# Kernel optimization log

Hardware: AMD Instinct MI355X
Metric: run time of the kernel (lower is better)

Reference implementation:

```python
import jax, jax.numpy as jnp
import numpy as np

B, DIN, NS, NF = 2048, 512, 256, 64

def setup_inputs() -> dict:
    key = jax.random.key(0)
    ks = jax.random.split(key, 16)
    s = 0.05
    return {
        'x_i': jax.random.normal(ks[0], (B, DIN), jnp.float32),
        'h_i': jax.random.normal(ks[1], (B, NS), jnp.float32),
        'S_i': jax.random.normal(ks[2], (B, 2, NS, NF), jnp.float32),
        'W_fste': jax.random.normal(ks[3], (DIN + NS, NS), jnp.float32) * s,
        'b_fste': jnp.zeros((NS,), jnp.float32),
        'W_ffreq': jax.random.normal(ks[4], (DIN + NS, NF), jnp.float32) * s,
        'b_ffreq': jnp.zeros((NF,), jnp.float32),
        'W_i': jax.random.normal(ks[5], (DIN + NS, NS), jnp.float32) * s,
        'b_i': jnp.zeros((NS,), jnp.float32),
        'W_c': jax.random.normal(ks[6], (DIN + NS, NS), jnp.float32) * s,
        'b_c': jnp.zeros((NS,), jnp.float32),
        'u_a': jax.random.normal(ks[7], (NF,), jnp.float32) * s,
        'b_a': jnp.zeros((NS,), jnp.float32),
        'W_o': jax.random.normal(ks[8], (DIN + NS + NS, NS), jnp.float32) * s,
        'b_o': jnp.zeros((NS,), jnp.float32),
        't': 3,
    }

def reference(x_i, h_i, S_i, W_fste, b_fste, W_ffreq, b_ffreq, W_i, b_i, W_c, b_c, u_a, b_a, W_o, b_o, t):
    nf = u_a.shape[0]
    # angle = ((arange(nf)*t) % nf) / (nf / (2*pi))  -- matches np precedence in source
    ang = ((jnp.arange(nf, dtype=jnp.float32) * t) % nf) * (2.0 * jnp.pi / nf)
    omega = jnp.stack([jnp.sin(ang), jnp.cos(ang)])[:, None]        # [2,1,nf]
    x_h = jnp.concatenate([x_i, h_i], axis=-1)                      # [B, DIN+NS]
    f_ste = jax.nn.sigmoid(x_h @ W_fste + b_fste)                   # [B,NS]
    f_freq = jax.nn.sigmoid(x_h @ W_ffreq + b_ffreq)                # [B,NF]
    F_t = jnp.einsum('bi,bj->bij', f_ste, f_freq)                   # [B,NS,NF]
    i_dot = jax.nn.sigmoid(x_h @ W_i + b_i)                         # [B,NS]
    c_wave = jnp.tanh(x_h @ W_c + b_c)                              # [B,NS]
    i_c_omega = (i_dot * c_wave)[:, None, :, None] * omega          # [B,2,NS,NF]
    S_next = S_i * F_t[:, None] + i_c_omega                         # [B,2,NS,NF]
    A_i = jnp.sqrt(jnp.sum(S_next ** 2, axis=1))                    # [B,NS,NF]
    c_t = jax.nn.sigmoid(jnp.einsum('bij,j->bi', A_i, u_a) + b_a)   # [B,NS]
    o_i = jax.nn.sigmoid(jnp.concatenate([x_h, c_t], -1) @ W_o + b_o)
    h_next = o_i * c_t
    return h_next, S_next
```

## Files before the change

kernel.cpp:

```cpp
#include <hip/hip_runtime.h>
#include <math.h>

#define BATCH 2048
#define DIN   512
#define NS    256
#define NF    64
#define KG    768
#define NG    832
#define NTOT  1088

__device__ __forceinline__ float sigmoidf_(float x) { return 1.0f / (1.0f + __expf(-x)); }

__global__ __launch_bounds__(256) void gates_gemm(
    const float* __restrict__ x, const float* __restrict__ h,
    const float* __restrict__ Wf, const float* __restrict__ bf,
    const float* __restrict__ Wq, const float* __restrict__ bq,
    const float* __restrict__ Wi, const float* __restrict__ bi,
    const float* __restrict__ Wc, const float* __restrict__ bcg,
    const float* __restrict__ Wo,
    float* __restrict__ gates, float* __restrict__ opart)
{
    __shared__ float As[2][32][68];
    __shared__ float Bs[2][32][68];

    const int nt = blockIdx.x;
    const int mt = blockIdx.y;
    const int t  = threadIdx.x;

    const int n0 = nt * 64;
    const float* Wp; const float* bp; int ld, noff, act;
    if (n0 < 256)      { Wp = Wf; bp = bf;  ld = 256; noff = 0;   act = 0; }
    else if (n0 < 320) { Wp = Wq; bp = bq;  ld = 64;  noff = 256; act = 0; }
    else if (n0 < 576) { Wp = Wi; bp = bi;  ld = 256; noff = 320; act = 0; }
    else if (n0 < 832) { Wp = Wc; bp = bcg; ld = 256; noff = 576; act = 1; }
    else               { Wp = Wo; bp = bf;  ld = 256; noff = 832; act = 2; }
    const int nloc0 = n0 - noff;

    const int tx = t & 15, ty = t >> 4;
    const int m0 = mt * 64;

    const int ar  = t & 63;
    const int ak0 = (t >> 6) * 8;
    const int brow  = t >> 3;
    const int bcol0 = (t & 7) * 8;

    const float* ax = x + (size_t)(m0 + ar) * DIN;
    const float* ah = h + (size_t)(m0 + ar) * NS;

    float acc[4][4] = {};
    float4 a0, a1, b0, b1;

    {
        const int k0 = ak0;
        a0 = *(const float4*)(ax + k0);
        a1 = *(const float4*)(ax + k0 + 4);
        const float* wr = Wp + (size_t)brow * ld + nloc0 + bcol0;
        b0 = *(const float4*)wr; b1 = *(const float4*)(wr + 4);
        As[0][ak0 + 0][ar] = a0.x; As[0][ak0 + 1][ar] = a0.y;
        As[0][ak0 + 2][ar] = a0.z; As[0][ak0 + 3][ar] = a0.w;
        As[0][ak0 + 4][ar] = a1.x; As[0][ak0 + 5][ar] = a1.y;
        As[0][ak0 + 6][ar] = a1.z; As[0][ak0 + 7][ar] = a1.w;
        *(float4*)&Bs[0][brow][bcol0]     = b0;
        *(float4*)&Bs[0][brow][bcol0 + 4] = b1;
    }
    __syncthreads();

    #pragma unroll 1
    for (int tI = 0; tI < 24; ++tI) {
        const int notlast = (tI < 23);
        if (notlast) {
            const int kt = (tI + 1) * 32;
            const int k0 = kt + ak0;
            a0 = (k0 < DIN)     ? *(const float4*)(ax + k0)
                                : *(const float4*)(ah + (k0 - DIN));
            a1 = (k0 + 4 < DIN) ? *(const float4*)(ax + k0 + 4)
                                : *(const float4*)(ah + (k0 + 4 - DIN));
            const float* wr = Wp + (size_t)(kt + brow) * ld + nloc0 + bcol0;
            b0 = *(const float4*)wr; b1 = *(const float4*)(wr + 4);
        }
        const float (*Asb)[68] = As[tI & 1];
        const float (*Bsb)[68] = Bs[tI & 1];
        #pragma unroll
        for (int kk = 0; kk < 32; ++kk) {
            const float4 a = *(const float4*)&Asb[kk][ty * 4];
            const float4 b = *(const float4*)&Bsb[kk][tx * 4];
            const float av[4] = { a.x, a.y, a.z, a.w };
            const float bv[4] = { b.x, b.y, b.z, b.w };
            #pragma unroll
            for (int r = 0; r < 4; ++r)
                #pragma unroll
                for (int c = 0; c < 4; ++c)
                    acc[r][c] = fmaf(av[r], bv[c], acc[r][c]);
        }
        if (notlast) {
            float (*Ad)[68] = As[(tI + 1) & 1];
            float (*Bd)[68] = Bs[(tI + 1) & 1];
            Ad[ak0 + 0][ar] = a0.x; Ad[ak0 + 1][ar] = a0.y;
            Ad[ak0 + 2][ar] = a0.z; Ad[ak0 + 3][ar] = a0.w;
            Ad[ak0 + 4][ar] = a1.x; Ad[ak0 + 5][ar] = a1.y;
            Ad[ak0 + 6][ar] = a1.z; Ad[ak0 + 7][ar] = a1.w;
            *(float4*)&Bd[brow][bcol0]     = b0;
            *(float4*)&Bd[brow][bcol0 + 4] = b1;
        }
        __syncthreads();
    }

    if (act == 2) {
        #pragma unroll
        for (int r = 0; r < 4; ++r) {
            const int m = m0 + ty * 4 + r;
            *(float4*)(opart + (size_t)m * NS + (n0 - 832) + tx * 4) =
                make_float4(acc[r][0], acc[r][1], acc[r][2], acc[r][3]);
        }
    } else {
        const float4 bb = *(const float4*)(bp + nloc0 + tx * 4);
        const float bvv[4] = { bb.x, bb.y, bb.z, bb.w };
        #pragma unroll
        for (int r = 0; r < 4; ++r) {
            const int m = m0 + ty * 4 + r;
            float o[4];
            #pragma unroll
            for (int c = 0; c < 4; ++c) {
                float v = acc[r][c] + bvv[c];
                o[c] = act ? tanhf(v) : sigmoidf_(v);
            }
            *(float4*)(gates + (size_t)m * NG + n0 + tx * 4) =
                make_float4(o[0], o[1], o[2], o[3]);
        }
    }
}

__global__ __launch_bounds__(256) void supdate(
    const float* __restrict__ S, const float* __restrict__ gates,
    const float* __restrict__ ua, const float* __restrict__ ba,
    const int* __restrict__ tptr,
    float* __restrict__ Sout, float* __restrict__ ct)
{
    const int tid = blockIdx.x * 256 + threadIdx.x;
    const int q    = tid & 15;
    const int pair = tid >> 4;
    const int b = pair >> 8, s = pair & 255;
    const int f0 = q * 4;
    const int tv = *tptr;

    const float* grow = gates + (size_t)b * NG;
    const float fste = grow[s];
    const float ic   = grow[320 + s] * grow[576 + s];

    const float4 ff  = *(const float4*)(grow + 256 + f0);
    const float4 ua4 = *(const float4*)(ua + f0);

    const size_t base0 = (((size_t)b * 2 + 0) * NS + s) * NF + f0;
    const size_t base1 = (((size_t)b * 2 + 1) * NS + s) * NF + f0;
    const float4 si0 = *(const float4*)(S + base0);
    const float4 si1 = *(const float4*)(S + base1);

    float fv[4] = { ff.x, ff.y, ff.z, ff.w };
    float uv[4] = { ua4.x, ua4.y, ua4.z, ua4.w };
    float a0[4] = { si0.x, si0.y, si0.z, si0.w };
    float a1[4] = { si1.x, si1.y, si1.z, si1.w };

    float part = 0.0f;
    float o0[4], o1[4];
    #pragma unroll
    for (int j = 0; j < 4; ++j) {
        int f = f0 + j;
        float ang = (float)((f * tv) & (NF - 1)) * (float)(M_PI / 32.0);
        float sn = __sinf(ang), cs = __cosf(ang);
        float F = fste * fv[j];
        float u = a0[j] * F + ic * sn;
        float v = a1[j] * F + ic * cs;
        o0[j] = u; o1[j] = v;
        part += sqrtf(u * u + v * v) * uv[j];
    }
    *(float4*)(Sout + base0) = make_float4(o0[0], o0[1], o0[2], o0[3]);
    *(float4*)(Sout + base1) = make_float4(o1[0], o1[1], o1[2], o1[3]);

    part += __shfl_xor(part, 1);
    part += __shfl_xor(part, 2);
    part += __shfl_xor(part, 4);
    part += __shfl_xor(part, 8);
    if (q == 0) ct[pair] = sigmoidf_(part + ba[s]);
}

__global__ __launch_bounds__(256) void out_gemm(
    const float* __restrict__ ct, const float* __restrict__ opart,
    const float* __restrict__ Wo, const float* __restrict__ bo,
    float* __restrict__ hout)
{
    __shared__ float As[2][32][36];
    __shared__ float Bs[2][32][68];

    const int t  = threadIdx.x;
    const int n0 = blockIdx.x * 64;
    const int m0 = blockIdx.y * 32;
    const int tx = t & 15, ty = t >> 4;

    const int ar  = t & 31;
    const int ak0 = (t >> 5) * 4;
    const int brow  = t >> 3;
    const int bcol0 = (t & 7) * 8;

    const float* Wp = Wo + (size_t)(DIN + NS) * NS;
    const float* act_row = ct + (size_t)(m0 + ar) * NS;

    float acc[2][4] = {};
    float4 a4, b0, b1;

    a4 = *(const float4*)(act_row + ak0);
    {
        const float* wr = Wp + (size_t)brow * NS + n0 + bcol0;
        b0 = *(const float4*)wr; b1 = *(const float4*)(wr + 4);
    }
    As[0][ak0 + 0][ar] = a4.x; As[0][ak0 + 1][ar] = a4.y;
    As[0][ak0 + 2][ar] = a4.z; As[0][ak0 + 3][ar] = a4.w;
    *(float4*)&Bs[0][brow][bcol0]     = b0;
    *(float4*)&Bs[0][brow][bcol0 + 4] = b1;
    __syncthreads();

    #pragma unroll 1
    for (int tI = 0; tI < 8; ++tI) {
        const int notlast = (tI < 7);
        if (notlast) {
            const int kt = (tI + 1) * 32;
            a4 = *(const float4*)(act_row + kt + ak0);
            const float* wr = Wp + (size_t)(kt + brow) * NS + n0 + bcol0;
            b0 = *(const float4*)wr; b1 = *(const float4*)(wr + 4);
        }
        const float (*Asb)[36] = As[tI & 1];
        const float (*Bsb)[68] = Bs[tI & 1];
        #pragma unroll
        for (int kk = 0; kk < 32; ++kk) {
            const float a0v = Asb[kk][ty * 2];
            const float a1v = Asb[kk][ty * 2 + 1];
            const float4 b = *(const float4*)&Bsb[kk][tx * 4];
            acc[0][0] = fmaf(a0v, b.x, acc[0][0]);
            acc[0][1] = fmaf(a0v, b.y, acc[0][1]);
            acc[0][2] = fmaf(a0v, b.z, acc[0][2]);
            acc[0][3] = fmaf(a0v, b.w, acc[0][3]);
            acc[1][0] = fmaf(a1v, b.x, acc[1][0]);
            acc[1][1] = fmaf(a1v, b.y, acc[1][1]);
            acc[1][2] = fmaf(a1v, b.z, acc[1][2]);
            acc[1][3] = fmaf(a1v, b.w, acc[1][3]);
        }
        if (notlast) {
            float (*Ad)[36] = As[(tI + 1) & 1];
            float (*Bd)[68] = Bs[(tI + 1) & 1];
            Ad[ak0 + 0][ar] = a4.x; Ad[ak0 + 1][ar] = a4.y;
            Ad[ak0 + 2][ar] = a4.z; Ad[ak0 + 3][ar] = a4.w;
            *(float4*)&Bd[brow][bcol0]     = b0;
            *(float4*)&Bd[brow][bcol0 + 4] = b1;
        }
        __syncthreads();
    }

    #pragma unroll
    for (int r = 0; r < 2; ++r) {
        const int m = m0 + ty * 2 + r;
        const float4 op = *(const float4*)(opart + (size_t)m * NS + n0 + tx * 4);
        const float4 bb = *(const float4*)(bo + n0 + tx * 4);
        const float4 cv = *(const float4*)(ct + (size_t)m * NS + n0 + tx * 4);
        float4 o;
        o.x = sigmoidf_(acc[r][0] + op.x + bb.x) * cv.x;
        o.y = sigmoidf_(acc[r][1] + op.y + bb.y) * cv.y;
        o.z = sigmoidf_(acc[r][2] + op.z + bb.z) * cv.z;
        o.w = sigmoidf_(acc[r][3] + op.w + bb.w) * cv.w;
        *(float4*)(hout + (size_t)m * NS + n0 + tx * 4) = o;
    }
}

extern "C" void kernel_launch(void* const* d_in, const int* in_sizes, int n_in,
                              void* d_out, int out_size, void* d_ws, size_t ws_size,
                              hipStream_t stream)
{
    const float* x  = (const float*)d_in[0];
    const float* h  = (const float*)d_in[1];
    const float* S  = (const float*)d_in[2];
    const float* Wf = (const float*)d_in[3];
    const float* bf = (const float*)d_in[4];
    const float* Wq = (const float*)d_in[5];
    const float* bq = (const float*)d_in[6];
    const float* Wi = (const float*)d_in[7];
    const float* bi = (const float*)d_in[8];
    const float* Wc = (const float*)d_in[9];
    const float* bc = (const float*)d_in[10];
    const float* ua = (const float*)d_in[11];
    const float* ba = (const float*)d_in[12];
    const float* Wo = (const float*)d_in[13];
    const float* bo = (const float*)d_in[14];
    const int*   tp = (const int*)d_in[15];

    float* gates = (float*)d_ws;
    float* ct    = gates + (size_t)BATCH * NG;
    float* opart = ct + (size_t)BATCH * NS;
    float* hout  = (float*)d_out;
    float* Sout  = hout + (size_t)BATCH * NS;

    gates_gemm<<<dim3(17, 32), 256, 0, stream>>>(x, h, Wf, bf, Wq, bq, Wi, bi, Wc, bc, Wo, gates, opart);
    supdate<<<dim3((BATCH * NS * 16) / 256), 256, 0, stream>>>(S, gates, ua, ba, tp, Sout, ct);
    out_gemm<<<dim3(4, 64), 256, 0, stream>>>(ct, opart, Wo, bo, hout);
}
```

Baseline: 594.1 us.

## Halve gates GEMM tile width and use nontemporal loads/stores for S

The gates GEMM now uses 64x32 tiles with 128-thread blocks, doubling the block count from 544 to 1088 to fill more of the GPU's compute units. The per-thread loaders are reworked so each thread loads 16 A elements and two strided B vectors. The S state update now reads and writes through nontemporal builtins, so the 268MB streaming traffic does not pollute the caches. The narrower tiles lower arithmetic intensity and add redundant A loads across N tiles.

```diff
diff --git a/kernel.cpp b/kernel.cpp
--- a/kernel.cpp
+++ b/kernel.cpp
@@ -9,9 +9,11 @@
 #define NG    832
 #define NTOT  1088
 
+typedef float v4f __attribute__((ext_vector_type(4)));
+
 __device__ __forceinline__ float sigmoidf_(float x) { return 1.0f / (1.0f + __expf(-x)); }
 
-__global__ __launch_bounds__(256) void gates_gemm(
+__global__ __launch_bounds__(128) void gates_gemm(
     const float* __restrict__ x, const float* __restrict__ h,
     const float* __restrict__ Wf, const float* __restrict__ bf,
     const float* __restrict__ Wq, const float* __restrict__ bq,
@@ -21,13 +23,13 @@
     float* __restrict__ gates, float* __restrict__ opart)
 {
     __shared__ float As[2][32][68];
-    __shared__ float Bs[2][32][68];
+    __shared__ float Bs[2][32][36];
 
     const int nt = blockIdx.x;
     const int mt = blockIdx.y;
     const int t  = threadIdx.x;
 
-    const int n0 = nt * 64;
+    const int n0 = nt * 32;
     const float* Wp; const float* bp; int ld, noff, act;
     if (n0 < 256)      { Wp = Wf; bp = bf;  ld = 256; noff = 0;   act = 0; }
     else if (n0 < 320) { Wp = Wq; bp = bq;  ld = 64;  noff = 256; act = 0; }
@@ -36,32 +38,37 @@
     else               { Wp = Wo; bp = bf;  ld = 256; noff = 832; act = 2; }
     const int nloc0 = n0 - noff;
 
-    const int tx = t & 15, ty = t >> 4;
+    const int tx = t & 7, ty = t >> 3;
     const int m0 = mt * 64;
 
     const int ar  = t & 63;
-    const int ak0 = (t >> 6) * 8;
-    const int brow  = t >> 3;
-    const int bcol0 = (t & 7) * 8;
+    const int ak0 = (t >> 6) * 16;
+    const int brow  = t >> 2;
+    const int bcol0 = (t & 3) * 4;
 
     const float* ax = x + (size_t)(m0 + ar) * DIN;
     const float* ah = h + (size_t)(m0 + ar) * NS;
 
     float acc[4][4] = {};
-    float4 a0, a1, b0, b1;
+    float4 a0, a1, a2, a3, b0, b1;
 
     {
-        const int k0 = ak0;
-        a0 = *(const float4*)(ax + k0);
-        a1 = *(const float4*)(ax + k0 + 4);
+        a0 = *(const float4*)(ax + ak0);
+        a1 = *(const float4*)(ax + ak0 + 4);
+        a2 = *(const float4*)(ax + ak0 + 8);
+        a3 = *(const float4*)(ax + ak0 + 12);
         const float* wr = Wp + (size_t)brow * ld + nloc0 + bcol0;
-        b0 = *(const float4*)wr; b1 = *(const float4*)(wr + 4);
-        As[0][ak0 + 0][ar] = a0.x; As[0][ak0 + 1][ar] = a0.y;
-        As[0][ak0 + 2][ar] = a0.z; As[0][ak0 + 3][ar] = a0.w;
-        As[0][ak0 + 4][ar] = a1.x; As[0][ak0 + 5][ar] = a1.y;
-        As[0][ak0 + 6][ar] = a1.z; As[0][ak0 + 7][ar] = a1.w;
-        *(float4*)&Bs[0][brow][bcol0]     = b0;
-        *(float4*)&Bs[0][brow][bcol0 + 4] = b1;
+        b0 = *(const float4*)wr; b1 = *(const float4*)(wr + 16);
+        As[0][ak0 +  0][ar] = a0.x; As[0][ak0 +  1][ar] = a0.y;
+        As[0][ak0 +  2][ar] = a0.z; As[0][ak0 +  3][ar] = a0.w;
+        As[0][ak0 +  4][ar] = a1.x; As[0][ak0 +  5][ar] = a1.y;
+        As[0][ak0 +  6][ar] = a1.z; As[0][ak0 +  7][ar] = a1.w;
+        As[0][ak0 +  8][ar] = a2.x; As[0][ak0 +  9][ar] = a2.y;
+        As[0][ak0 + 10][ar] = a2.z; As[0][ak0 + 11][ar] = a2.w;
+        As[0][ak0 + 12][ar] = a3.x; As[0][ak0 + 13][ar] = a3.y;
+        As[0][ak0 + 14][ar] = a3.z; As[0][ak0 + 15][ar] = a3.w;
+        *(float4*)&Bs[0][brow][bcol0]      = b0;
+        *(float4*)&Bs[0][brow][bcol0 + 16] = b1;
     }
     __syncthreads();
 
@@ -71,15 +78,16 @@
         if (notlast) {
             const int kt = (tI + 1) * 32;
             const int k0 = kt + ak0;
-            a0 = (k0 < DIN)     ? *(const float4*)(ax + k0)
-                                : *(const float4*)(ah + (k0 - DIN));
-            a1 = (k0 + 4 < DIN) ? *(const float4*)(ax + k0 + 4)
-                                : *(const float4*)(ah + (k0 + 4 - DIN));
+            const float* ap = (k0 < DIN) ? (ax + k0) : (ah + (k0 - DIN));
+            a0 = *(const float4*)(ap);
+            a1 = *(const float4*)(ap + 4);
+            a2 = *(const float4*)(ap + 8);
+            a3 = *(const float4*)(ap + 12);
             const float* wr = Wp + (size_t)(kt + brow) * ld + nloc0 + bcol0;
-            b0 = *(const float4*)wr; b1 = *(const float4*)(wr + 4);
+            b0 = *(const float4*)wr; b1 = *(const float4*)(wr + 16);
         }
         const float (*Asb)[68] = As[tI & 1];
-        const float (*Bsb)[68] = Bs[tI & 1];
+        const float (*Bsb)[36] = Bs[tI & 1];
         #pragma unroll
         for (int kk = 0; kk < 32; ++kk) {
             const float4 a = *(const float4*)&Asb[kk][ty * 4];
@@ -94,13 +102,17 @@
         }
         if (notlast) {
             float (*Ad)[68] = As[(tI + 1) & 1];
-            float (*Bd)[68] = Bs[(tI + 1) & 1];
-            Ad[ak0 + 0][ar] = a0.x; Ad[ak0 + 1][ar] = a0.y;
-            Ad[ak0 + 2][ar] = a0.z; Ad[ak0 + 3][ar] = a0.w;
-            Ad[ak0 + 4][ar] = a1.x; Ad[ak0 + 5][ar] = a1.y;
-            Ad[ak0 + 6][ar] = a1.z; Ad[ak0 + 7][ar] = a1.w;
-            *(float4*)&Bd[brow][bcol0]     = b0;
-            *(float4*)&Bd[brow][bcol0 + 4] = b1;
+            float (*Bd)[36] = Bs[(tI + 1) & 1];
+            Ad[ak0 +  0][ar] = a0.x; Ad[ak0 +  1][ar] = a0.y;
+            Ad[ak0 +  2][ar] = a0.z; Ad[ak0 +  3][ar] = a0.w;
+            Ad[ak0 +  4][ar] = a1.x; Ad[ak0 +  5][ar] = a1.y;
+            Ad[ak0 +  6][ar] = a1.z; Ad[ak0 +  7][ar] = a1.w;
+            Ad[ak0 +  8][ar] = a2.x; Ad[ak0 +  9][ar] = a2.y;
+            Ad[ak0 + 10][ar] = a2.z; Ad[ak0 + 11][ar] = a2.w;
+            Ad[ak0 + 12][ar] = a3.x; Ad[ak0 + 13][ar] = a3.y;
+            Ad[ak0 + 14][ar] = a3.z; Ad[ak0 + 15][ar] = a3.w;
+            *(float4*)&Bd[brow][bcol0]      = b0;
+            *(float4*)&Bd[brow][bcol0 + 16] = b1;
         }
         __syncthreads();
     }
@@ -152,8 +164,8 @@
 
     const size_t base0 = (((size_t)b * 2 + 0) * NS + s) * NF + f0;
     const size_t base1 = (((size_t)b * 2 + 1) * NS + s) * NF + f0;
-    const float4 si0 = *(const float4*)(S + base0);
-    const float4 si1 = *(const float4*)(S + base1);
+    const v4f si0 = __builtin_nontemporal_load((const v4f*)(S + base0));
+    const v4f si1 = __builtin_nontemporal_load((const v4f*)(S + base1));
 
     float fv[4] = { ff.x, ff.y, ff.z, ff.w };
     float uv[4] = { ua4.x, ua4.y, ua4.z, ua4.w };
@@ -161,7 +173,7 @@
     float a1[4] = { si1.x, si1.y, si1.z, si1.w };
 
     float part = 0.0f;
-    float o0[4], o1[4];
+    v4f o0, o1;
     #pragma unroll
     for (int j = 0; j < 4; ++j) {
         int f = f0 + j;
@@ -173,8 +185,8 @@
         o0[j] = u; o1[j] = v;
         part += sqrtf(u * u + v * v) * uv[j];
     }
-    *(float4*)(Sout + base0) = make_float4(o0[0], o0[1], o0[2], o0[3]);
-    *(float4*)(Sout + base1) = make_float4(o1[0], o1[1], o1[2], o1[3]);
+    __builtin_nontemporal_store(o0, (v4f*)(Sout + base0));
+    __builtin_nontemporal_store(o1, (v4f*)(Sout + base1));
 
     part += __shfl_xor(part, 1);
     part += __shfl_xor(part, 2);
@@ -296,7 +308,7 @@
     float* hout  = (float*)d_out;
     float* Sout  = hout + (size_t)BATCH * NS;
 
-    gates_gemm<<<dim3(17, 32), 256, 0, stream>>>(x, h, Wf, bf, Wq, bq, Wi, bi, Wc, bc, Wo, gates, opart);
+    gates_gemm<<<dim3(34, 32), 128, 0, stream>>>(x, h, Wf, bf, Wq, bq, Wi, bi, Wc, bc, Wo, gates, opart);
     supdate<<<dim3((BATCH * NS * 16) / 256), 256, 0, stream>>>(S, gates, ua, ba, tp, Sout, ct);
     out_gemm<<<dim3(4, 64), 256, 0, stream>>>(ct, opart, Wo, bo, hout);
 }
```

After: 588.1 us. No clear change (-1.0%).
